# Kernel tuning notes

Hardware: AMD Instinct MI355X
Metric: run time of the kernel (lower is better)

## Reference

```python
import jax, jax.numpy as jnp
import numpy as np

N = 4096      # num_nodes
F = 16        # num_features
K = 3         # diffusion steps


def _diffusion_powers(W):
    """Replicates __init__: powers of (DO^-1 W) and (DI^-1 W^T), k=0..K-1."""
    out_deg = W.sum(axis=1)            # W @ ones
    in_deg = W.sum(axis=0)             # W.T @ ones
    A = W / out_deg[:, None]           # DO_inv @ W
    B = W.T / in_deg[:, None]          # DI_inv @ W.T
    eye = jnp.eye(N, dtype=W.dtype)
    Wp, WTp, Pa, Pb = [], [], eye, eye
    for _ in range(K):
        Wp.append(Pa)
        WTp.append(Pb)
        Pa = Pa @ A
        Pb = Pb @ B
    return jnp.stack(Wp), jnp.stack(WTp)   # each [K, N, N]


def setup_inputs() -> dict:
    key = jax.random.key(0)
    k1, k2, k3 = jax.random.split(key, 3)
    W = jax.random.uniform(k1, (N, N), dtype=jnp.float32)  # random adjacency, like np.random.rand
    Wp, WTp = _diffusion_powers(W)
    X = jax.random.normal(k2, (N, F), dtype=jnp.float32)
    theta = jax.random.normal(k3, (K, 2), dtype=jnp.float32)
    return {"X": X, "theta": theta, "Wp": Wp, "WTp": WTp}


def reference(X, theta, Wp, WTp):
    # Original: for each feature p and step k,
    #   X_out[:, p] += (theta[k,0]*Wp[k] + theta[k,1]*WTp[k]) @ X[:, p]
    # The feature loop is a columnwise matmul; fuse the k-sum into one matrix M.
    M = jnp.einsum('k,knm->nm', theta[:, 0], Wp) + jnp.einsum('k,knm->nm', theta[:, 1], WTp)
    return X + M @ X
```

## Files before the change

kernel.cpp:

```cpp
#include <hip/hip_runtime.h>


constexpr int N  = 4096;
constexpr int F  = 16;
constexpr int TM = 8;
constexpr int TK = 128;
constexpr int KS = 4;
constexpr int XP = F + 4;

typedef float floatx4 __attribute__((ext_vector_type(4)));

__device__ __forceinline__ float4 nt_load4(const float* p) {
    floatx4 v = __builtin_nontemporal_load((const floatx4*)p);
    return make_float4(v.x, v.y, v.z, v.w);
}

__global__ __launch_bounds__(256) void init_out_kernel(
    const float* __restrict__ X,
    const float* __restrict__ theta,
    float* __restrict__ out)
{
    const float self_scale = 1.0f + theta[0] + theta[1];
    const int i = blockIdx.x * blockDim.x + threadIdx.x;
    if (i < N * F / 4) {
        float4 x = ((const float4*)X)[i];
        x.x *= self_scale; x.y *= self_scale; x.z *= self_scale; x.w *= self_scale;
        ((float4*)out)[i] = x;
    }
}

__global__ __launch_bounds__(256) void diffconv_kernel(
    const float* __restrict__ X,
    const float* __restrict__ theta,
    const float* __restrict__ Wp,
    const float* __restrict__ WTp,
    float* __restrict__ out)
{
    __shared__ float c_lds[TM][TK];
    __shared__ float x_lds[TK][XP];
    __shared__ float red_lds[4][TM][F];

    const int t    = threadIdx.x;
    const int row0 = blockIdx.x * TM;
    const int kbeg = blockIdx.y * (N / KS);

    const float th10 = theta[2], th11 = theta[3];
    const float th20 = theta[4], th21 = theta[5];

    const float* __restrict__ Wp1  = Wp  + (size_t)N * N;
    const float* __restrict__ Wp2  = Wp  + 2 * (size_t)N * N;
    const float* __restrict__ WTp1 = WTp + (size_t)N * N;
    const float* __restrict__ WTp2 = WTp + 2 * (size_t)N * N;

    const int sr = t >> 5;
    const int sc = (t & 31) << 2;

    const int xr0 = t >> 2;
    const int xc0 = (t & 3) << 2;
    const int xr1 = (t + 256) >> 2;
    const int xc1 = xc0;

    const int f0 = (t & 3) << 2;
    const int m0 = (t >> 2) << 1;

    float acc[TM][4];
#pragma unroll
    for (int r = 0; r < TM; ++r)
#pragma unroll
        for (int j = 0; j < 4; ++j) acc[r][j] = 0.0f;

    constexpr int NIT = N / KS / TK;

    size_t moff = (size_t)(row0 + sr) * N + (size_t)(kbeg + sc);
    float4 a0 = nt_load4(Wp1  + moff);
    float4 a1 = nt_load4(WTp1 + moff);
    float4 a2 = nt_load4(Wp2  + moff);
    float4 a3 = nt_load4(WTp2 + moff);
    float4 xv0 = *(const float4*)(X + (size_t)(kbeg + xr0) * F + xc0);
    float4 xv1 = *(const float4*)(X + (size_t)(kbeg + xr1) * F + xc1);

    for (int it = 0; it < NIT; ++it) {
        float4 c4;
        c4.x = th10*a0.x + th11*a1.x + th20*a2.x + th21*a3.x;
        c4.y = th10*a0.y + th11*a1.y + th20*a2.y + th21*a3.y;
        c4.z = th10*a0.z + th11*a1.z + th20*a2.z + th21*a3.z;
        c4.w = th10*a0.w + th11*a1.w + th20*a2.w + th21*a3.w;
        *(float4*)&c_lds[sr][sc] = c4;
        *(float4*)&x_lds[xr0][xc0] = xv0;
        *(float4*)&x_lds[xr1][xc1] = xv1;
        __syncthreads();

        if (it + 1 < NIT) {
            const int kb = kbeg + (it + 1) * TK;
            moff = (size_t)(row0 + sr) * N + (size_t)(kb + sc);
            a0 = nt_load4(Wp1  + moff);
            a1 = nt_load4(WTp1 + moff);
            a2 = nt_load4(Wp2  + moff);
            a3 = nt_load4(WTp2 + moff);
            xv0 = *(const float4*)(X + (size_t)(kb + xr0) * F + xc0);
            xv1 = *(const float4*)(X + (size_t)(kb + xr1) * F + xc1);
        }

        const float4 x0 = *(const float4*)&x_lds[m0][f0];
        const float4 x1 = *(const float4*)&x_lds[m0 + 1][f0];
#pragma unroll
        for (int r = 0; r < TM; ++r) {
            const float2 c = *(const float2*)&c_lds[r][m0];
            acc[r][0] = fmaf(c.x, x0.x, fmaf(c.y, x1.x, acc[r][0]));
            acc[r][1] = fmaf(c.x, x0.y, fmaf(c.y, x1.y, acc[r][1]));
            acc[r][2] = fmaf(c.x, x0.z, fmaf(c.y, x1.z, acc[r][2]));
            acc[r][3] = fmaf(c.x, x0.w, fmaf(c.y, x1.w, acc[r][3]));
        }
        __syncthreads();
    }

#pragma unroll
    for (int mask = 4; mask <= 32; mask <<= 1) {
#pragma unroll
        for (int r = 0; r < TM; ++r)
#pragma unroll
            for (int j = 0; j < 4; ++j)
                acc[r][j] += __shfl_xor(acc[r][j], mask, 64);
    }

    const int wave = t >> 6;
    const int lane = t & 63;
    if (lane < 4) {
#pragma unroll
        for (int r = 0; r < TM; ++r)
#pragma unroll
            for (int j = 0; j < 4; ++j)
                red_lds[wave][r][lane * 4 + j] = acc[r][j];
    }
    __syncthreads();

    if (t < TM * F) {
        const int r = t >> 4;
        const int f = t & 15;
        const float s = red_lds[0][r][f] + red_lds[1][r][f]
                      + red_lds[2][r][f] + red_lds[3][r][f];
        atomicAdd(&out[(size_t)(row0 + r) * F + f], s);
    }
}

extern "C" void kernel_launch(void* const* d_in, const int* in_sizes, int n_in,
                              void* d_out, int out_size, void* d_ws, size_t ws_size,
                              hipStream_t stream) {
    const float* X     = (const float*)d_in[0];
    const float* theta = (const float*)d_in[1];
    const float* Wp    = (const float*)d_in[2];
    const float* WTp   = (const float*)d_in[3];
    float* out = (float*)d_out;

    init_out_kernel<<<(N * F / 4 + 255) / 256, 256, 0, stream>>>(X, theta, out);

    dim3 grid(N / TM, KS);
    diffconv_kernel<<<grid, 256, 0, stream>>>(X, theta, Wp, WTp, out);
}
```

Measured before the change: 348.2 us.

## Restructure to one row per wave with full-K pass and fused epilogue

```diff
diff --git a/kernel.cpp b/kernel.cpp
--- a/kernel.cpp
+++ b/kernel.cpp
@@ -3,47 +3,25 @@
 
 constexpr int N  = 4096;
 constexpr int F  = 16;
-constexpr int TM = 8;
-constexpr int TK = 128;
-constexpr int KS = 4;
-constexpr int XP = F + 4;
+constexpr int TPB     = 512;
+constexpr int RPB     = 8;
+constexpr int PHASE_K = 1024;
 
-typedef float floatx4 __attribute__((ext_vector_type(4)));
-
-__device__ __forceinline__ float4 nt_load4(const float* p) {
-    floatx4 v = __builtin_nontemporal_load((const floatx4*)p);
-    return make_float4(v.x, v.y, v.z, v.w);
-}
-
-__global__ __launch_bounds__(256) void init_out_kernel(
-    const float* __restrict__ X,
-    const float* __restrict__ theta,
-    float* __restrict__ out)
-{
-    const float self_scale = 1.0f + theta[0] + theta[1];
-    const int i = blockIdx.x * blockDim.x + threadIdx.x;
-    if (i < N * F / 4) {
-        float4 x = ((const float4*)X)[i];
-        x.x *= self_scale; x.y *= self_scale; x.z *= self_scale; x.w *= self_scale;
-        ((float4*)out)[i] = x;
-    }
-}
-
-__global__ __launch_bounds__(256) void diffconv_kernel(
+__global__ __launch_bounds__(TPB, 4) void diffconv_kernel(
     const float* __restrict__ X,
     const float* __restrict__ theta,
     const float* __restrict__ Wp,
     const float* __restrict__ WTp,
     float* __restrict__ out)
 {
-    __shared__ float c_lds[TM][TK];
-    __shared__ float x_lds[TK][XP];
-    __shared__ float red_lds[4][TM][F];
+    __shared__ float x_lds[PHASE_K * F];
 
-    const int t    = threadIdx.x;
-    const int row0 = blockIdx.x * TM;
-    const int kbeg = blockIdx.y * (N / KS);
+    const int tid  = threadIdx.x;
+    const int lane = tid & 63;
+    const int wave = tid >> 6;
+    const int r    = blockIdx.x * RPB + wave;
 
+    const float th00 = theta[0], th01 = theta[1];
     const float th10 = theta[2], th11 = theta[3];
     const float th20 = theta[4], th21 = theta[5];
 
@@ -52,94 +30,92 @@
     const float* __restrict__ WTp1 = WTp + (size_t)N * N;
     const float* __restrict__ WTp2 = WTp + 2 * (size_t)N * N;
 
-    const int sr = t >> 5;
-    const int sc = (t & 31) << 2;
+    const size_t rowb = (size_t)r * N;
 
-    const int xr0 = t >> 2;
-    const int xc0 = (t & 3) << 2;
-    const int xr1 = (t + 256) >> 2;
-    const int xc1 = xc0;
+    float acc[16];
+#pragma unroll
+    for (int f = 0; f < 16; ++f) acc[f] = 0.0f;
 
-    const int f0 = (t & 3) << 2;
-    const int m0 = (t >> 2) << 1;
+    float bufA[4][4], bufB[4][4];
 
-    float acc[TM][4];
+    auto prefetch = [&](float (&dst)[4][4], int k0) {
 #pragma unroll
-    for (int r = 0; r < TM; ++r)
+        for (int j = 0; j < 4; ++j) {
+            const size_t o = rowb + (size_t)(k0 + j * 64 + lane);
+            dst[0][j] = __builtin_nontemporal_load(Wp1  + o);
+            dst[1][j] = __builtin_nontemporal_load(WTp1 + o);
+            dst[2][j] = __builtin_nontemporal_load(Wp2  + o);
+            dst[3][j] = __builtin_nontemporal_load(WTp2 + o);
+        }
+    };
+
+    auto compute = [&](float (&cur)[4][4], int k0) {
 #pragma unroll
-        for (int j = 0; j < 4; ++j) acc[r][j] = 0.0f;
+        for (int j = 0; j < 4; ++j) {
+            const float c = th10 * cur[0][j] + th11 * cur[1][j]
+                          + th20 * cur[2][j] + th21 * cur[3][j];
+            const int krel = (k0 & (PHASE_K - 1)) + j * 64 + lane;
+            const int base = krel << 4;
+            const int sw   = (krel >> 1) & 3;
+#pragma unroll
+            for (int q = 0; q < 4; ++q) {
+                const float4 xq = *(const float4*)&x_lds[base + ((q ^ sw) << 2)];
+                acc[4*q+0] = fmaf(c, xq.x, acc[4*q+0]);
+                acc[4*q+1] = fmaf(c, xq.y, acc[4*q+1]);
+                acc[4*q+2] = fmaf(c, xq.z, acc[4*q+2]);
+                acc[4*q+3] = fmaf(c, xq.w, acc[4*q+3]);
+            }
+        }
+    };
 
-    constexpr int NIT = N / KS / TK;
+    prefetch(bufA, 0);
 
-    size_t moff = (size_t)(row0 + sr) * N + (size_t)(kbeg + sc);
-    float4 a0 = nt_load4(Wp1  + moff);
-    float4 a1 = nt_load4(WTp1 + moff);
-    float4 a2 = nt_load4(Wp2  + moff);
-    float4 a3 = nt_load4(WTp2 + moff);
-    float4 xv0 = *(const float4*)(X + (size_t)(kbeg + xr0) * F + xc0);
-    float4 xv1 = *(const float4*)(X + (size_t)(kbeg + xr1) * F + xc1);
-
-    for (int it = 0; it < NIT; ++it) {
-        float4 c4;
-        c4.x = th10*a0.x + th11*a1.x + th20*a2.x + th21*a3.x;
-        c4.y = th10*a0.y + th11*a1.y + th20*a2.y + th21*a3.y;
-        c4.z = th10*a0.z + th11*a1.z + th20*a2.z + th21*a3.z;
-        c4.w = th10*a0.w + th11*a1.w + th20*a2.w + th21*a3.w;
-        *(float4*)&c_lds[sr][sc] = c4;
-        *(float4*)&x_lds[xr0][xc0] = xv0;
-        *(float4*)&x_lds[xr1][xc1] = xv1;
+    for (int p = 0; p < 4; ++p) {
+        __syncthreads();
+#pragma unroll
+        for (int h = 0; h < 2; ++h) {
+            const int krel = tid + h * 512;
+            const float4* src =
+                (const float4*)(X + (size_t)(p * PHASE_K + krel) * F);
+            const int base = krel << 4;
+            const int sw   = (krel >> 1) & 3;
+#pragma unroll
+            for (int q = 0; q < 4; ++q)
+                *(float4*)&x_lds[base + ((q ^ sw) << 2)] = src[q];
+        }
         __syncthreads();
 
-        if (it + 1 < NIT) {
-            const int kb = kbeg + (it + 1) * TK;
-            moff = (size_t)(row0 + sr) * N + (size_t)(kb + sc);
-            a0 = nt_load4(Wp1  + moff);
-            a1 = nt_load4(WTp1 + moff);
-            a2 = nt_load4(Wp2  + moff);
-            a3 = nt_load4(WTp2 + moff);
-            xv0 = *(const float4*)(X + (size_t)(kb + xr0) * F + xc0);
-            xv1 = *(const float4*)(X + (size_t)(kb + xr1) * F + xc1);
-        }
-
-        const float4 x0 = *(const float4*)&x_lds[m0][f0];
-        const float4 x1 = *(const float4*)&x_lds[m0 + 1][f0];
-#pragma unroll
-        for (int r = 0; r < TM; ++r) {
-            const float2 c = *(const float2*)&c_lds[r][m0];
-            acc[r][0] = fmaf(c.x, x0.x, fmaf(c.y, x1.x, acc[r][0]));
-            acc[r][1] = fmaf(c.x, x0.y, fmaf(c.y, x1.y, acc[r][1]));
-            acc[r][2] = fmaf(c.x, x0.z, fmaf(c.y, x1.z, acc[r][2]));
-            acc[r][3] = fmaf(c.x, x0.w, fmaf(c.y, x1.w, acc[r][3]));
-        }
-        __syncthreads();
+        const int k0 = p * PHASE_K;
+        prefetch(bufB, k0 + 256);
+        compute(bufA, k0);
+        prefetch(bufA, k0 + 512);
+        compute(bufB, k0 + 256);
+        prefetch(bufB, k0 + 768);
+        compute(bufA, k0 + 512);
+        if (p < 3) prefetch(bufA, k0 + 1024);
+        compute(bufB, k0 + 768);
     }
 
 #pragma unroll
-    for (int mask = 4; mask <= 32; mask <<= 1) {
+    for (int mask = 1; mask < 64; mask <<= 1)
 #pragma unroll
-        for (int r = 0; r < TM; ++r)
+        for (int f = 0; f < 16; ++f)
+            acc[f] += __shfl_xor(acc[f], mask, 64);
+
+    if (lane == 0) {
+        const float self_scale = 1.0f + th00 + th01;
+        const float4* xp = (const float4*)(X + (size_t)r * F);
+        float4*       op = (float4*)(out + (size_t)r * F);
 #pragma unroll
-            for (int j = 0; j < 4; ++j)
-                acc[r][j] += __shfl_xor(acc[r][j], mask, 64);
-    }
-
-    const int wave = t >> 6;
-    const int lane = t & 63;
-    if (lane < 4) {
-#pragma unroll
-        for (int r = 0; r < TM; ++r)
-#pragma unroll
-            for (int j = 0; j < 4; ++j)
-                red_lds[wave][r][lane * 4 + j] = acc[r][j];
-    }
-    __syncthreads();
-
-    if (t < TM * F) {
-        const int r = t >> 4;
-        const int f = t & 15;
-        const float s = red_lds[0][r][f] + red_lds[1][r][f]
-                      + red_lds[2][r][f] + red_lds[3][r][f];
-        atomicAdd(&out[(size_t)(row0 + r) * F + f], s);
+        for (int q = 0; q < 4; ++q) {
+            const float4 xv = xp[q];
+            float4 ov;
+            ov.x = self_scale * xv.x + acc[4*q+0];
+            ov.y = self_scale * xv.y + acc[4*q+1];
+            ov.z = self_scale * xv.z + acc[4*q+2];
+            ov.w = self_scale * xv.w + acc[4*q+3];
+            op[q] = ov;
+        }
     }
 }
 
@@ -152,8 +128,5 @@
     const float* WTp   = (const float*)d_in[3];
     float* out = (float*)d_out;
 
-    init_out_kernel<<<(N * F / 4 + 255) / 256, 256, 0, stream>>>(X, theta, out);
-
-    dim3 grid(N / TM, KS);
-    diffconv_kernel<<<grid, 256, 0, stream>>>(X, theta, Wp, WTp, out);
+    diffconv_kernel<<<N / RPB, TPB, 0, stream>>>(X, theta, Wp, WTp, out);
 }
```

After: 615.9 us. +76.9%, slower.
